# Optimization experiments

Measured on AMD Instinct MI355X. Metric: run time of the kernel, lower is better.

Reference implementation:

```python
import jax, jax.numpy as jnp
import numpy as np

B, N, C, H = 8, 1024, 384, 6
D = C // H
SPAN = C  # att_span = pos_ebd_size = dim (module sets max_relative_positions = dim)
SCALE_FACTOR = 3  # 1 + c2p + p2c


def setup_inputs() -> dict:
    key = jax.random.key(0)
    ks = jax.random.split(key, 10)
    w = lambda k, shp: jax.random.normal(k, shp, jnp.float32) * 0.02
    rel_pos = (jnp.arange(N)[:, None] - jnp.arange(N)[None, :]).astype(jnp.int32)
    return {
        "x": jax.random.normal(ks[0], (B, N, C), jnp.float32),
        "relative_pos": rel_pos,
        "rel_embeddings": jax.random.normal(ks[1], (2 * SPAN, C), jnp.float32) * 0.02,
        "Wq": w(ks[2], (C, C)), "bq": jnp.zeros((C,), jnp.float32),
        "Wk": w(ks[3], (C, C)), "bk": jnp.zeros((C,), jnp.float32),
        "Wv": w(ks[4], (C, C)), "bv": jnp.zeros((C,), jnp.float32),
        "Wpk": w(ks[5], (C, C)), "bpk": jnp.zeros((C,), jnp.float32),
        "Wpq": w(ks[6], (C, C)), "bpq": jnp.zeros((C,), jnp.float32),
        "Wo": w(ks[7], (C, C)), "bo": jnp.zeros((C,), jnp.float32),
    }


def reference(x, relative_pos, rel_embeddings, Wq, bq, Wk, bk, Wv, bv,
              Wpk, bpk, Wpq, bpq, Wo, bo):
    Bx, Nx, Cx = x.shape
    # content projections -> (B, H, N, D)
    q = (x @ Wq + bq).reshape(Bx, Nx, H, D).transpose(0, 2, 1, 3)
    k = (x @ Wk + bk).reshape(Bx, Nx, H, D).transpose(0, 2, 1, 3)
    v = (x @ Wv + bv).reshape(Bx, Nx, H, D).transpose(0, 2, 1, 3)
    scale = jnp.sqrt(jnp.asarray(D * SCALE_FACTOR, jnp.float32))
    attn = jnp.einsum('bhnd,bhmd->bhnm', q, k) / scale  # (B,H,N,N)

    # positional projections of rel_embeddings[0:2*SPAN] -> (H, 2*SPAN, D)
    pos_k = (rel_embeddings @ Wpk + bpk).reshape(2 * SPAN, H, D).transpose(1, 0, 2)
    pos_q = (rel_embeddings @ Wpq + bpq).reshape(2 * SPAN, H, D).transpose(1, 0, 2)

    rp = relative_pos.astype(jnp.int32)
    # content->position: gather columns of q @ pos_k^T by bucketed index
    c2p_pos = jnp.clip(rp + SPAN, 0, 2 * SPAN - 1)  # (N,N)
    c2p = jnp.einsum('bhnd,hpd->bhnp', q, pos_k)    # (B,H,N,2*SPAN)
    c2p = jnp.take_along_axis(
        c2p, jnp.broadcast_to(c2p_pos[None, None], (Bx, H, Nx, Nx)), axis=-1)

    # position->content: gather columns of k @ pos_q^T, then transpose
    p2c_pos = jnp.clip(-rp + SPAN, 0, 2 * SPAN - 1)
    p2c = jnp.einsum('bhnd,hpd->bhnp', k, pos_q)    # (B,H,N,2*SPAN)
    p2c = jnp.take_along_axis(
        p2c, jnp.broadcast_to(p2c_pos[None, None], (Bx, H, Nx, Nx)), axis=-1)
    p2c = jnp.swapaxes(p2c, -1, -2)

    attn = attn + (c2p + p2c) / scale
    probs = jax.nn.softmax(attn, axis=-1)
    out = jnp.einsum('bhnm,bhmd->bhnd', probs, v)
    out = out.transpose(0, 2, 1, 3).reshape(Bx, Nx, Cx)
    return out @ Wo + bo
```

## Files before the change

### kernel.cpp

```cpp
#include <hip/hip_runtime.h>
#include <math.h>

typedef __attribute__((ext_vector_type(8))) short short8;
typedef __attribute__((ext_vector_type(4))) float v4f;
typedef __attribute__((ext_vector_type(4))) unsigned short us4;

#define INV_SCALE 0.07216878364870322f

__device__ __forceinline__ unsigned short f2bf(float f) {
  unsigned u = __builtin_bit_cast(unsigned, f);
  u = (u + 0x7FFFu + ((u >> 16) & 1u)) >> 16;
  return (unsigned short)u;
}
__device__ __forceinline__ float bf2f(unsigned short h) {
  unsigned u = ((unsigned)h) << 16;
  return __builtin_bit_cast(float, u);
}

enum { OM_PLAIN = 0, OM_Q = 1, OM_K = 2, OM_VT = 3, OM_PK = 4, OM_PQ = 5 };

__global__ __launch_bounds__(256) void cvt_bf16(
    const float* __restrict__ x, const float* __restrict__ re,
    unsigned short* __restrict__ xb, unsigned short* __restrict__ reb) {
  size_t idx = ((size_t)blockIdx.x * 256 + threadIdx.x) * 8;
  const float* src;
  unsigned short* dst;
  if (idx < 3145728) {
    src = x + idx; dst = xb + idx;
  } else {
    size_t r = idx - 3145728;
    if (r >= 294912) return;
    src = re + r; dst = reb + r;
  }
  float4 u0 = *(const float4*)src;
  float4 u1 = *(const float4*)(src + 4);
  short8 v;
  v[0] = (short)f2bf(u0.x); v[1] = (short)f2bf(u0.y);
  v[2] = (short)f2bf(u0.z); v[3] = (short)f2bf(u0.w);
  v[4] = (short)f2bf(u1.x); v[5] = (short)f2bf(u1.y);
  v[6] = (short)f2bf(u1.z); v[7] = (short)f2bf(u1.w);
  *(short8*)dst = v;
}

__global__ __launch_bounds__(256) void transpose_w(
    const float* __restrict__ Wq, const float* __restrict__ Wk,
    const float* __restrict__ Wv, const float* __restrict__ Wpk,
    const float* __restrict__ Wpq, const float* __restrict__ Wo,
    unsigned short* __restrict__ Wt) {
  __shared__ unsigned short Ts[64][68];
  const int mat = blockIdx.y;
  const float* W = mat == 0 ? Wq : mat == 1 ? Wk : mat == 2 ? Wv
                 : mat == 3 ? Wpk : mat == 4 ? Wpq : Wo;
  const int tk = (blockIdx.x % 6) * 64, tn = (blockIdx.x / 6) * 64;
  const int t = threadIdx.x;
#pragma unroll
  for (int it = 0; it < 4; ++it) {
    int r = (t >> 4) + it * 16, c = (t & 15) * 4;
    float4 v = *(const float4*)(W + (size_t)(tk + r) * 384 + tn + c);
    us4 p = {f2bf(v.x), f2bf(v.y), f2bf(v.z), f2bf(v.w)};
    *(us4*)&Ts[r][c] = p;
  }
  __syncthreads();
  unsigned short* out = Wt + (size_t)mat * 147456;
#pragma unroll
  for (int it = 0; it < 2; ++it) {
    int n = (t >> 3) + it * 32, kc = (t & 7) * 8;
    unsigned short tmp[8];
#pragma unroll
    for (int j = 0; j < 8; ++j) tmp[j] = Ts[kc + j][n];
    *(short8*)(out + (size_t)(tn + n) * 384 + tk + kc) = *(short8*)tmp;
  }
}

template <int OMODE, int NP>
__device__ __forceinline__ void pgemm_body(
    const unsigned short* __restrict__ A, const unsigned short* __restrict__ Bt,
    const float* __restrict__ bias, void* __restrict__ out,
    int m0, int ng0, float scale, unsigned short (*Bs)[392]) {
  const int t = threadIdx.x;
  const int lane = t & 63, w = t >> 6, li = lane & 15, quad = lane >> 4;
  const int row = m0 + w * 16 + li;
  const int sr = t >> 2, scq = (t & 3) * 96;

#pragma unroll
  for (int i = 0; i < 12; ++i)
    *(short8*)&Bs[sr][scq + i * 8] =
        *(const short8*)(Bt + (size_t)(ng0 * 64 + sr) * 384 + scq + i * 8);

  short8 afr[12];
#pragma unroll
  for (int kk = 0; kk < 12; ++kk)
    afr[kk] = *(const short8*)(A + (size_t)row * 384 + kk * 32 + quad * 8);

#pragma unroll
  for (int pp = 0; pp < NP; ++pp) {
    __syncthreads();
    v4f acc[4] = {};
#pragma unroll
    for (int kk = 0; kk < 12; ++kk) {
#pragma unroll
      for (int nt = 0; nt < 4; ++nt) {
        short8 bf = *(const short8*)&Bs[nt * 16 + li][kk * 32 + quad * 8];
        acc[nt] = __builtin_amdgcn_mfma_f32_16x16x32_bf16(afr[kk], bf, acc[nt], 0, 0, 0);
      }
    }
    __syncthreads();
    if (pp + 1 < NP) {
#pragma unroll
      for (int i = 0; i < 12; ++i)
        *(short8*)&Bs[sr][scq + i * 8] =
            *(const short8*)(Bt + (size_t)((ng0 + pp + 1) * 64 + sr) * 384 + scq + i * 8);
    }
    const int n0 = (ng0 + pp) * 64;
#pragma unroll
    for (int nt = 0; nt < 4; ++nt) {
      int col = n0 + nt * 16 + li;
      float bv = bias[col];
      int h = col >> 6, d = col & 63;
#pragma unroll
      for (int i = 0; i < 4; ++i) {
        int orow = m0 + w * 16 + quad * 4 + i;
        float val = (acc[nt][i] + bv) * scale;
        if constexpr (OMODE == OM_PLAIN) {
          ((float*)out)[(size_t)orow * 384 + col] = val;
        } else if constexpr (OMODE == OM_Q || OMODE == OM_K) {
          int b = orow >> 10, n = orow & 1023;
          ((unsigned short*)out)[((size_t)(b * 6 + h) << 16) + (n << 6) + d] = f2bf(val);
        } else if constexpr (OMODE == OM_VT) {
          int b = orow >> 10, n = orow & 1023;
          ((unsigned short*)out)[((size_t)(b * 6 + h) << 16) + (d << 10) + n] = f2bf(val);
        } else {
          ((unsigned short*)out)[(size_t)h * 49152 + (size_t)orow * 64 + d] = f2bf(val);
        }
      }
    }
  }
}

__global__ __launch_bounds__(256, 3) void proj_all(
    const unsigned short* __restrict__ xb, const unsigned short* __restrict__ reb,
    const unsigned short* __restrict__ Wt,
    const float* __restrict__ bq, const float* __restrict__ bk,
    const float* __restrict__ bv, const float* __restrict__ bpk,
    const float* __restrict__ bpq,
    unsigned short* __restrict__ qw, unsigned short* __restrict__ kw,
    unsigned short* __restrict__ vtw, unsigned short* __restrict__ pkw,
    unsigned short* __restrict__ pqw) {
  __shared__ __align__(16) unsigned short Bs[64][392];
  const int y = blockIdx.y;
  const int m0 = blockIdx.x * 64;
  int which, ng0;
  if (y < 6) {
    which = y >> 1; ng0 = (y & 1) * 3;
  } else {
    int p = y - 6;
    which = 3 + (p >> 1); ng0 = (p & 1) * 3;
    if (m0 >= 768) return;
  }
  const unsigned short* A = which < 3 ? xb : reb;
  const unsigned short* Bt = Wt + (size_t)which * 147456;
  switch (which) {
    case 0: pgemm_body<OM_Q, 3>(A, Bt, bq,  qw,  m0, ng0, INV_SCALE, Bs); break;
    case 1: pgemm_body<OM_K, 3>(A, Bt, bk,  kw,  m0, ng0, 1.f, Bs); break;
    case 2: pgemm_body<OM_VT,3>(A, Bt, bv,  vtw, m0, ng0, 1.f, Bs); break;
    case 3: pgemm_body<OM_PK,3>(A, Bt, bpk, pkw, m0, ng0, 1.f, Bs); break;
    default: pgemm_body<OM_PQ,3>(A, Bt, bpq, pqw, m0, ng0, INV_SCALE, Bs); break;
  }
}

__global__ __launch_bounds__(256, 3) void out_gemm(
    const unsigned short* __restrict__ ao, const unsigned short* __restrict__ Bt,
    const float* __restrict__ bo, float* __restrict__ out) {
  __shared__ __align__(16) unsigned short Bs[64][392];
  pgemm_body<OM_PLAIN, 3>(ao, Bt, bo, out,
                          blockIdx.x * 64, blockIdx.y * 3, 1.f, Bs);
}

#define ASTR 72

__global__ __launch_bounds__(256, 3) void attn_fused(
    const unsigned short* __restrict__ q, const unsigned short* __restrict__ k,
    const unsigned short* __restrict__ vt, const unsigned short* __restrict__ pk,
    const unsigned short* __restrict__ pq, unsigned short* __restrict__ ao) {
  __shared__ __align__(16) unsigned short band1[128][ASTR];
  __shared__ __align__(16) unsigned short band2[128][ASTR];
  __shared__ __align__(16) unsigned short Ps[64][ASTR];

  const int f = blockIdx.x + (blockIdx.y << 4);
  const int g = f & 7, s = f >> 3;
  const int bh = g * 6 + (s >> 4);
  const int n0 = (s & 15) * 64;
  const int h = bh % 6, b = bh / 6;
  const int t = threadIdx.x;
  const int lane = t & 63, w = t >> 6;
  const int li = lane & 15, quad = lane >> 4;

  const unsigned short* qb = q + ((size_t)bh << 16);
  const unsigned short* kb = k + ((size_t)bh << 16);
  const unsigned short* vb = vt + ((size_t)bh << 16);
  const unsigned short* pkh = pk + (size_t)h * 49152;
  const unsigned short* pqh = pq + (size_t)h * 49152;

  short8 aq0 = *(const short8*)(qb + (size_t)(n0 + w * 16 + li) * 64 + quad * 8);
  short8 aq1 = *(const short8*)(qb + (size_t)(n0 + w * 16 + li) * 64 + 32 + quad * 8);

  float l_part[4] = {0.f, 0.f, 0.f, 0.f};
  v4f o[4] = {};

  const int sr = t >> 1, sc = (t & 1) * 32;
  short8 st1[4], st2[4];
  {
    int src = n0 - 0 - 63 + 384 + sr;
    src = src < 0 ? 0 : (src > 767 ? 767 : src);
    const unsigned short* p1 = pkh + (size_t)src * 64 + sc;
    const unsigned short* p2 = pqh + (size_t)src * 64 + sc;
#pragma unroll
    for (int ss = 0; ss < 4; ++ss) {
      st1[ss] = *(const short8*)(p1 + ss * 8);
      st2[ss] = *(const short8*)(p2 + ss * 8);
    }
  }

  for (int j0 = 0; j0 < 1024; j0 += 64) {
    __syncthreads();
#pragma unroll
    for (int ss = 0; ss < 4; ++ss) {
      *(short8*)&band1[sr][sc + ss * 8] = st1[ss];
      *(short8*)&band2[sr][sc + ss * 8] = st2[ss];
    }
    __syncthreads();

    {
      int src = n0 - (j0 + 64) - 63 + 384 + sr;
      src = src < 0 ? 0 : (src > 767 ? 767 : src);
      const unsigned short* p1 = pkh + (size_t)src * 64 + sc;
      const unsigned short* p2 = pqh + (size_t)src * 64 + sc;
#pragma unroll
      for (int ss = 0; ss < 4; ++ss) {
        st1[ss] = *(const short8*)(p1 + ss * 8);
        st2[ss] = *(const short8*)(p2 + ss * 8);
      }
    }

    short8 ak0 = *(const short8*)(kb + (size_t)(j0 + w * 16 + li) * 64 + quad * 8);
    short8 ak1 = *(const short8*)(kb + (size_t)(j0 + w * 16 + li) * 64 + 32 + quad * 8);

    v4f t1a[8] = {}, t2a[8] = {};
#pragma unroll
    for (int ct = 0; ct < 8; ++ct) {
      short8 b10 = *(const short8*)&band1[ct * 16 + li][quad * 8];
      short8 b11 = *(const short8*)&band1[ct * 16 + li][32 + quad * 8];
      t1a[ct] = __builtin_amdgcn_mfma_f32_16x16x32_bf16(aq0, b10, t1a[ct], 0, 0, 0);
      t1a[ct] = __builtin_amdgcn_mfma_f32_16x16x32_bf16(aq1, b11, t1a[ct], 0, 0, 0);
      short8 b20 = *(const short8*)&band2[ct * 16 + li][quad * 8];
      short8 b21 = *(const short8*)&band2[ct * 16 + li][32 + quad * 8];
      t2a[ct] = __builtin_amdgcn_mfma_f32_16x16x32_bf16(ak0, b20, t2a[ct], 0, 0, 0);
      t2a[ct] = __builtin_amdgcn_mfma_f32_16x16x32_bf16(ak1, b21, t2a[ct], 0, 0, 0);
    }
    __syncthreads();

#pragma unroll
    for (int ct = 0; ct < 8; ++ct) {
      us4 p1 = {f2bf(t1a[ct][0]), f2bf(t1a[ct][1]), f2bf(t1a[ct][2]), f2bf(t1a[ct][3])};
      us4 p2 = {f2bf(t2a[ct][0]), f2bf(t2a[ct][1]), f2bf(t2a[ct][2]), f2bf(t2a[ct][3])};
      *(us4*)&band1[ct * 16 + li][w * 16 + quad * 4] = p1;
      *(us4*)&band2[ct * 16 + li][w * 16 + quad * 4] = p2;
    }
    v4f sqk[4] = {};
#pragma unroll
    for (int nt = 0; nt < 4; ++nt) {
      short8 b0 = *(const short8*)(kb + (size_t)(j0 + nt * 16 + li) * 64 + quad * 8);
      short8 b1 = *(const short8*)(kb + (size_t)(j0 + nt * 16 + li) * 64 + 32 + quad * 8);
      sqk[nt] = __builtin_amdgcn_mfma_f32_16x16x32_bf16(aq0, b0, sqk[nt], 0, 0, 0);
      sqk[nt] = __builtin_amdgcn_mfma_f32_16x16x32_bf16(aq1, b1, sqk[nt], 0, 0, 0);
    }
    __syncthreads();

#pragma unroll
    for (int nt = 0; nt < 4; ++nt) {
      int jl = nt * 16 + li;
#pragma unroll
      for (int i = 0; i < 4; ++i) {
        int nl = w * 16 + quad * 4 + i;
        int r = nl - jl + 63;
        float s2 = sqk[nt][i] + bf2f(band1[r][nl]) + bf2f(band2[r][jl]);
        float p = __expf(s2);
        l_part[i] += p;
        Ps[nl][jl] = f2bf(p);
      }
    }
#pragma unroll
    for (int kst = 0; kst < 2; ++kst) {
      short8 ap = *(const short8*)&Ps[w * 16 + li][kst * 32 + quad * 8];
#pragma unroll
      for (int nt = 0; nt < 4; ++nt) {
        short8 bv2 = *(const short8*)(vb + (size_t)(nt * 16 + li) * 1024 + j0 + kst * 32 + quad * 8);
        o[nt] = __builtin_amdgcn_mfma_f32_16x16x32_bf16(ap, bv2, o[nt], 0, 0, 0);
      }
    }
  }

#pragma unroll
  for (int i = 0; i < 4; ++i) {
    float l = l_part[i];
    l += __shfl_xor(l, 1);
    l += __shfl_xor(l, 2);
    l += __shfl_xor(l, 4);
    l += __shfl_xor(l, 8);
    float inv_l = 1.f / l;
    int nl = w * 16 + quad * 4 + i;
#pragma unroll
    for (int nt = 0; nt < 4; ++nt)
      ao[((size_t)(b * 1024 + n0 + nl)) * 384 + h * 64 + nt * 16 + li] =
          f2bf(o[nt][i] * inv_l);
  }
}

extern "C" void kernel_launch(void* const* d_in, const int* in_sizes, int n_in,
                              void* d_out, int out_size, void* d_ws,
                              size_t ws_size, hipStream_t stream) {
  const float* x   = (const float*)d_in[0];
  const float* re  = (const float*)d_in[2];
  const float* Wq  = (const float*)d_in[3];
  const float* bq  = (const float*)d_in[4];
  const float* Wk  = (const float*)d_in[5];
  const float* bk  = (const float*)d_in[6];
  const float* Wv  = (const float*)d_in[7];
  const float* bv  = (const float*)d_in[8];
  const float* Wpk = (const float*)d_in[9];
  const float* bpk = (const float*)d_in[10];
  const float* Wpq = (const float*)d_in[11];
  const float* bpq = (const float*)d_in[12];
  const float* Wo  = (const float*)d_in[13];
  const float* bo  = (const float*)d_in[14];
  float* out = (float*)d_out;

  unsigned short* ws = (unsigned short*)d_ws;
  unsigned short* Wt  = ws;
  unsigned short* qw  = Wt + 884736;
  unsigned short* kw  = qw + 3145728;
  unsigned short* vtw = kw + 3145728;
  unsigned short* pkw = vtw + 3145728;
  unsigned short* pqw = pkw + 294912;
  unsigned short* aow = pqw + 294912;
  unsigned short* xb  = aow + 3145728;
  unsigned short* reb = xb + 3145728;

  cvt_bf16<<<dim3(1680), 256, 0, stream>>>(x, re, xb, reb);
  transpose_w<<<dim3(36, 6), 256, 0, stream>>>(Wq, Wk, Wv, Wpk, Wpq, Wo, Wt);
  proj_all<<<dim3(128, 10), 256, 0, stream>>>(xb, reb, Wt, bq, bk, bv, bpk, bpq,
                                              qw, kw, vtw, pkw, pqw);
  attn_fused<<<dim3(16, 48), 256, 0, stream>>>(qw, kw, vtw, pkw, pqw, aow);
  out_gemm<<<dim3(128, 2), 256, 0, stream>>>(aow, Wt + 5 * 147456, bo, out);
}
```

Measured before the change: 260.4 us.

## Fuse all stages into one persistent kernel with atomic grid barriers

Replaces five separate launches (convert, weight transpose, projections, attention, output GEMM) with a single 768-block kernel. The stages are separated by software grid barriers built on a global atomic counter, which is zeroed by a memset. The aim is to remove launch overhead and inter-kernel gaps. In exchange, the barriers need all 768 blocks to be co-resident (3 per CU), and the projection stage becomes unbalanced because the first 48 blocks also compute the positional projections.

```diff
diff --git a/kernel.cpp b/kernel.cpp
--- a/kernel.cpp
+++ b/kernel.cpp
@@ -6,6 +6,7 @@
 typedef __attribute__((ext_vector_type(4))) unsigned short us4;
 
 #define INV_SCALE 0.07216878364870322f
+#define NBLK 768u
 
 __device__ __forceinline__ unsigned short f2bf(float f) {
   unsigned u = __builtin_bit_cast(unsigned, f);
@@ -19,63 +20,22 @@
 
 enum { OM_PLAIN = 0, OM_Q = 1, OM_K = 2, OM_VT = 3, OM_PK = 4, OM_PQ = 5 };
 
-__global__ __launch_bounds__(256) void cvt_bf16(
-    const float* __restrict__ x, const float* __restrict__ re,
-    unsigned short* __restrict__ xb, unsigned short* __restrict__ reb) {
-  size_t idx = ((size_t)blockIdx.x * 256 + threadIdx.x) * 8;
-  const float* src;
-  unsigned short* dst;
-  if (idx < 3145728) {
-    src = x + idx; dst = xb + idx;
-  } else {
-    size_t r = idx - 3145728;
-    if (r >= 294912) return;
-    src = re + r; dst = reb + r;
-  }
-  float4 u0 = *(const float4*)src;
-  float4 u1 = *(const float4*)(src + 4);
-  short8 v;
-  v[0] = (short)f2bf(u0.x); v[1] = (short)f2bf(u0.y);
-  v[2] = (short)f2bf(u0.z); v[3] = (short)f2bf(u0.w);
-  v[4] = (short)f2bf(u1.x); v[5] = (short)f2bf(u1.y);
-  v[6] = (short)f2bf(u1.z); v[7] = (short)f2bf(u1.w);
-  *(short8*)dst = v;
-}
-
-__global__ __launch_bounds__(256) void transpose_w(
-    const float* __restrict__ Wq, const float* __restrict__ Wk,
-    const float* __restrict__ Wv, const float* __restrict__ Wpk,
-    const float* __restrict__ Wpq, const float* __restrict__ Wo,
-    unsigned short* __restrict__ Wt) {
-  __shared__ unsigned short Ts[64][68];
-  const int mat = blockIdx.y;
-  const float* W = mat == 0 ? Wq : mat == 1 ? Wk : mat == 2 ? Wv
-                 : mat == 3 ? Wpk : mat == 4 ? Wpq : Wo;
-  const int tk = (blockIdx.x % 6) * 64, tn = (blockIdx.x / 6) * 64;
-  const int t = threadIdx.x;
-#pragma unroll
-  for (int it = 0; it < 4; ++it) {
-    int r = (t >> 4) + it * 16, c = (t & 15) * 4;
-    float4 v = *(const float4*)(W + (size_t)(tk + r) * 384 + tn + c);
-    us4 p = {f2bf(v.x), f2bf(v.y), f2bf(v.z), f2bf(v.w)};
-    *(us4*)&Ts[r][c] = p;
-  }
+__device__ __forceinline__ void gbar(unsigned* cnt, int t) {
+  __threadfence();
   __syncthreads();
-  unsigned short* out = Wt + (size_t)mat * 147456;
-#pragma unroll
-  for (int it = 0; it < 2; ++it) {
-    int n = (t >> 3) + it * 32, kc = (t & 7) * 8;
-    unsigned short tmp[8];
-#pragma unroll
-    for (int j = 0; j < 8; ++j) tmp[j] = Ts[kc + j][n];
-    *(short8*)(out + (size_t)(tn + n) * 384 + tk + kc) = *(short8*)tmp;
-  }
-}
-
-template <int OMODE, int NP>
-__device__ __forceinline__ void pgemm_body(
+  if (t == 0) {
+    __hip_atomic_fetch_add(cnt, 1u, __ATOMIC_ACQ_REL, __HIP_MEMORY_SCOPE_AGENT);
+    while (__hip_atomic_load(cnt, __ATOMIC_ACQUIRE, __HIP_MEMORY_SCOPE_AGENT) < NBLK)
+      __builtin_amdgcn_s_sleep(2);
+  }
+  __syncthreads();
+  __threadfence();
+}
+
+template <int OMODE>
+__device__ __forceinline__ void pgemm_task(
     const unsigned short* __restrict__ A, const unsigned short* __restrict__ Bt,
-    const float* __restrict__ bias, void* __restrict__ out,
+    const float* __restrict__ bias, void* __restrict__ outp,
     int m0, int ng0, float scale, unsigned short (*Bs)[392]) {
   const int t = threadIdx.x;
   const int lane = t & 63, w = t >> 6, li = lane & 15, quad = lane >> 4;
@@ -93,7 +53,7 @@
     afr[kk] = *(const short8*)(A + (size_t)row * 384 + kk * 32 + quad * 8);
 
 #pragma unroll
-  for (int pp = 0; pp < NP; ++pp) {
+  for (int pp = 0; pp < 3; ++pp) {
     __syncthreads();
     v4f acc[4] = {};
 #pragma unroll
@@ -105,7 +65,7 @@
       }
     }
     __syncthreads();
-    if (pp + 1 < NP) {
+    if (pp + 1 < 3) {
 #pragma unroll
       for (int i = 0; i < 12; ++i)
         *(short8*)&Bs[sr][scq + i * 8] =
@@ -122,71 +82,32 @@
         int orow = m0 + w * 16 + quad * 4 + i;
         float val = (acc[nt][i] + bv) * scale;
         if constexpr (OMODE == OM_PLAIN) {
-          ((float*)out)[(size_t)orow * 384 + col] = val;
+          ((float*)outp)[(size_t)orow * 384 + col] = val;
         } else if constexpr (OMODE == OM_Q || OMODE == OM_K) {
           int b = orow >> 10, n = orow & 1023;
-          ((unsigned short*)out)[((size_t)(b * 6 + h) << 16) + (n << 6) + d] = f2bf(val);
+          ((unsigned short*)outp)[((size_t)(b * 6 + h) << 16) + (n << 6) + d] = f2bf(val);
         } else if constexpr (OMODE == OM_VT) {
           int b = orow >> 10, n = orow & 1023;
-          ((unsigned short*)out)[((size_t)(b * 6 + h) << 16) + (d << 10) + n] = f2bf(val);
+          ((unsigned short*)outp)[((size_t)(b * 6 + h) << 16) + (d << 10) + n] = f2bf(val);
         } else {
-          ((unsigned short*)out)[(size_t)h * 49152 + (size_t)orow * 64 + d] = f2bf(val);
+          ((unsigned short*)outp)[(size_t)h * 49152 + (size_t)orow * 64 + d] = f2bf(val);
         }
       }
     }
   }
 }
 
-__global__ __launch_bounds__(256, 3) void proj_all(
-    const unsigned short* __restrict__ xb, const unsigned short* __restrict__ reb,
-    const unsigned short* __restrict__ Wt,
-    const float* __restrict__ bq, const float* __restrict__ bk,
-    const float* __restrict__ bv, const float* __restrict__ bpk,
-    const float* __restrict__ bpq,
-    unsigned short* __restrict__ qw, unsigned short* __restrict__ kw,
-    unsigned short* __restrict__ vtw, unsigned short* __restrict__ pkw,
-    unsigned short* __restrict__ pqw) {
-  __shared__ __align__(16) unsigned short Bs[64][392];
-  const int y = blockIdx.y;
-  const int m0 = blockIdx.x * 64;
-  int which, ng0;
-  if (y < 6) {
-    which = y >> 1; ng0 = (y & 1) * 3;
-  } else {
-    int p = y - 6;
-    which = 3 + (p >> 1); ng0 = (p & 1) * 3;
-    if (m0 >= 768) return;
-  }
-  const unsigned short* A = which < 3 ? xb : reb;
-  const unsigned short* Bt = Wt + (size_t)which * 147456;
-  switch (which) {
-    case 0: pgemm_body<OM_Q, 3>(A, Bt, bq,  qw,  m0, ng0, INV_SCALE, Bs); break;
-    case 1: pgemm_body<OM_K, 3>(A, Bt, bk,  kw,  m0, ng0, 1.f, Bs); break;
-    case 2: pgemm_body<OM_VT,3>(A, Bt, bv,  vtw, m0, ng0, 1.f, Bs); break;
-    case 3: pgemm_body<OM_PK,3>(A, Bt, bpk, pkw, m0, ng0, 1.f, Bs); break;
-    default: pgemm_body<OM_PQ,3>(A, Bt, bpq, pqw, m0, ng0, INV_SCALE, Bs); break;
-  }
-}
-
-__global__ __launch_bounds__(256, 3) void out_gemm(
-    const unsigned short* __restrict__ ao, const unsigned short* __restrict__ Bt,
-    const float* __restrict__ bo, float* __restrict__ out) {
-  __shared__ __align__(16) unsigned short Bs[64][392];
-  pgemm_body<OM_PLAIN, 3>(ao, Bt, bo, out,
-                          blockIdx.x * 64, blockIdx.y * 3, 1.f, Bs);
-}
-
 #define ASTR 72
 
-__global__ __launch_bounds__(256, 3) void attn_fused(
-    const unsigned short* __restrict__ q, const unsigned short* __restrict__ k,
+__device__ __forceinline__ void attn_task(
+    int f, const unsigned short* __restrict__ q, const unsigned short* __restrict__ k,
     const unsigned short* __restrict__ vt, const unsigned short* __restrict__ pk,
-    const unsigned short* __restrict__ pq, unsigned short* __restrict__ ao) {
-  __shared__ __align__(16) unsigned short band1[128][ASTR];
-  __shared__ __align__(16) unsigned short band2[128][ASTR];
-  __shared__ __align__(16) unsigned short Ps[64][ASTR];
-
-  const int f = blockIdx.x + (blockIdx.y << 4);
+    const unsigned short* __restrict__ pq, unsigned short* __restrict__ ao,
+    unsigned short* smem) {
+  unsigned short (*band1)[ASTR] = (unsigned short(*)[ASTR])smem;
+  unsigned short (*band2)[ASTR] = (unsigned short(*)[ASTR])(smem + 128 * ASTR);
+  unsigned short (*Ps)[ASTR]    = (unsigned short(*)[ASTR])(smem + 256 * ASTR);
+
   const int g = f & 7, s = f >> 3;
   const int bh = g * 6 + (s >> 4);
   const int n0 = (s & 15) * 64;
@@ -313,6 +234,114 @@
     for (int nt = 0; nt < 4; ++nt)
       ao[((size_t)(b * 1024 + n0 + nl)) * 384 + h * 64 + nt * 16 + li] =
           f2bf(o[nt][i] * inv_l);
+  }
+}
+
+__global__ __launch_bounds__(256, 3) void fused_all(
+    const float* __restrict__ x, const float* __restrict__ re,
+    const float* __restrict__ Wq, const float* __restrict__ bq,
+    const float* __restrict__ Wk, const float* __restrict__ bk,
+    const float* __restrict__ Wv, const float* __restrict__ bv,
+    const float* __restrict__ Wpk, const float* __restrict__ bpk,
+    const float* __restrict__ Wpq, const float* __restrict__ bpq,
+    const float* __restrict__ Wo, const float* __restrict__ bo,
+    float* __restrict__ out, unsigned short* __restrict__ ws,
+    unsigned* __restrict__ cnt) {
+  __shared__ __align__(16) unsigned short smem[25088];
+
+  unsigned short* Wt  = ws;
+  unsigned short* qw  = Wt + 884736;
+  unsigned short* kw  = qw + 3145728;
+  unsigned short* vtw = kw + 3145728;
+  unsigned short* pkw = vtw + 3145728;
+  unsigned short* pqw = pkw + 294912;
+  unsigned short* aow = pqw + 294912;
+  unsigned short* xb  = aow + 3145728;
+  unsigned short* reb = xb + 3145728;
+
+  const int f = blockIdx.x;
+  const int t = threadIdx.x;
+
+  {
+    size_t idx = ((size_t)f * 256 + t) * 16;
+    float4 u0 = *(const float4*)(x + idx);
+    float4 u1 = *(const float4*)(x + idx + 4);
+    float4 u2 = *(const float4*)(x + idx + 8);
+    float4 u3 = *(const float4*)(x + idx + 12);
+    short8 v0, v1;
+    v0[0] = (short)f2bf(u0.x); v0[1] = (short)f2bf(u0.y);
+    v0[2] = (short)f2bf(u0.z); v0[3] = (short)f2bf(u0.w);
+    v0[4] = (short)f2bf(u1.x); v0[5] = (short)f2bf(u1.y);
+    v0[6] = (short)f2bf(u1.z); v0[7] = (short)f2bf(u1.w);
+    v1[0] = (short)f2bf(u2.x); v1[1] = (short)f2bf(u2.y);
+    v1[2] = (short)f2bf(u2.z); v1[3] = (short)f2bf(u2.w);
+    v1[4] = (short)f2bf(u3.x); v1[5] = (short)f2bf(u3.y);
+    v1[6] = (short)f2bf(u3.z); v1[7] = (short)f2bf(u3.w);
+    *(short8*)(xb + idx) = v0;
+    *(short8*)(xb + idx + 8) = v1;
+  }
+  if (f >= 216 && f < 360) {
+    size_t r = ((size_t)(f - 216) * 256 + t) * 8;
+    float4 u0 = *(const float4*)(re + r);
+    float4 u1 = *(const float4*)(re + r + 4);
+    short8 v;
+    v[0] = (short)f2bf(u0.x); v[1] = (short)f2bf(u0.y);
+    v[2] = (short)f2bf(u0.z); v[3] = (short)f2bf(u0.w);
+    v[4] = (short)f2bf(u1.x); v[5] = (short)f2bf(u1.y);
+    v[6] = (short)f2bf(u1.z); v[7] = (short)f2bf(u1.w);
+    *(short8*)(reb + r) = v;
+  }
+  if (f < 216) {
+    const int mat = f / 36, rem = f % 36;
+    const float* W = mat == 0 ? Wq : mat == 1 ? Wk : mat == 2 ? Wv
+                   : mat == 3 ? Wpk : mat == 4 ? Wpq : Wo;
+    const int tk = (rem % 6) * 64, tn = (rem / 6) * 64;
+    unsigned short (*Ts)[68] = (unsigned short(*)[68])smem;
+#pragma unroll
+    for (int it = 0; it < 4; ++it) {
+      int r = (t >> 4) + it * 16, c = (t & 15) * 4;
+      float4 v = *(const float4*)(W + (size_t)(tk + r) * 384 + tn + c);
+      us4 p = {f2bf(v.x), f2bf(v.y), f2bf(v.z), f2bf(v.w)};
+      *(us4*)&Ts[r][c] = p;
+    }
+    __syncthreads();
+    unsigned short* outp = Wt + (size_t)mat * 147456;
+#pragma unroll
+    for (int it = 0; it < 2; ++it) {
+      int n = (t >> 3) + it * 32, kc = (t & 7) * 8;
+      unsigned short tmp[8];
+#pragma unroll
+      for (int j = 0; j < 8; ++j) tmp[j] = Ts[kc + j][n];
+      *(short8*)(outp + (size_t)(tn + n) * 384 + tk + kc) = *(short8*)tmp;
+    }
+  }
+  gbar(cnt + 0, t);
+
+  {
+    unsigned short (*Bs)[392] = (unsigned short(*)[392])smem;
+    const int which = f / 256, r = f & 255;
+    const int m0 = (r >> 1) * 64, ng0 = (r & 1) * 3;
+    switch (which) {
+      case 0:  pgemm_task<OM_Q >(xb, Wt,              bq, qw,  m0, ng0, INV_SCALE, Bs); break;
+      case 1:  pgemm_task<OM_K >(xb, Wt + 147456,     bk, kw,  m0, ng0, 1.f, Bs); break;
+      default: pgemm_task<OM_VT>(xb, Wt + 2 * 147456, bv, vtw, m0, ng0, 1.f, Bs); break;
+    }
+    if (f < 48) {
+      const int u = f % 24;
+      const int m2 = (u >> 1) * 64, ng2 = (u & 1) * 3;
+      if (f < 24) pgemm_task<OM_PK>(reb, Wt + 3 * 147456, bpk, pkw, m2, ng2, 1.f, Bs);
+      else        pgemm_task<OM_PQ>(reb, Wt + 4 * 147456, bpq, pqw, m2, ng2, INV_SCALE, Bs);
+    }
+  }
+  gbar(cnt + 1, t);
+
+  attn_task(f, qw, kw, vtw, pkw, pqw, aow, smem);
+  gbar(cnt + 2, t);
+
+  if (f < 256) {
+    unsigned short (*Bs)[392] = (unsigned short(*)[392])smem;
+    pgemm_task<OM_PLAIN>(aow, Wt + 5 * 147456, bo, out,
+                         (f >> 1) * 64, (f & 1) * 3, 1.f, Bs);
   }
 }
 
@@ -336,20 +365,10 @@
   float* out = (float*)d_out;
 
   unsigned short* ws = (unsigned short*)d_ws;
-  unsigned short* Wt  = ws;
-  unsigned short* qw  = Wt + 884736;
-  unsigned short* kw  = qw + 3145728;
-  unsigned short* vtw = kw + 3145728;
-  unsigned short* pkw = vtw + 3145728;
-  unsigned short* pqw = pkw + 294912;
-  unsigned short* aow = pqw + 294912;
-  unsigned short* xb  = aow + 3145728;
-  unsigned short* reb = xb + 3145728;
-
-  cvt_bf16<<<dim3(1680), 256, 0, stream>>>(x, re, xb, reb);
-  transpose_w<<<dim3(36, 6), 256, 0, stream>>>(Wq, Wk, Wv, Wpk, Wpq, Wo, Wt);
-  proj_all<<<dim3(128, 10), 256, 0, stream>>>(xb, reb, Wt, bq, bk, bv, bpk, bpq,
-                                              qw, kw, vtw, pkw, pqw);
-  attn_fused<<<dim3(16, 48), 256, 0, stream>>>(qw, kw, vtw, pkw, pqw, aow);
-  out_gemm<<<dim3(128, 2), 256, 0, stream>>>(aow, Wt + 5 * 147456, bo, out);
-}
+  unsigned* cnt = (unsigned*)(ws + 884736 + 3 * 3145728 + 2 * 294912 +
+                              3145728 + 3145728 + 294912);
+  hipMemsetAsync(cnt, 0, 16, stream);
+  fused_all<<<dim3(NBLK), dim3(256), 0, stream>>>(
+      x, re, Wq, bq, Wk, bk, Wv, bv, Wpk, bpk, Wpq, bpq, Wo, bo,
+      out, ws, cnt);
+}
```

Measured after the change: 982.4 us. +277.3%, slower.
